# Kernel tuning notes

Measured on AMD Instinct MI355X. Metric: run time of the kernel, lower is better.

Reference implementation:

```python
import jax, jax.numpy as jnp
import numpy as np

DT = 1.0
EPS = 1e-12
BETA_MIN = 1e-4

def setup_inputs() -> dict:
    key = jax.random.key(0)
    k1, k2 = jax.random.split(key, 2)
    B, W, M, F = 32, 32, 4096, 8
    H = 256
    feature = jax.random.uniform(k1, (B, W, M, F), jnp.float32) * 1000.0
    N = jax.random.uniform(k2, (M,), jnp.float32, minval=1e5, maxval=1e6)
    # tanh-reparam params: (tanh(x)+1)/2 = p  ->  x = atanh(2p-1)
    logbeta = jnp.asarray(np.arctanh(2.0 * 0.3 - 1.0), jnp.float32)
    loggamma = jnp.asarray(np.arctanh(2.0 * 0.1 - 1.0), jnp.float32)
    return {"feature": feature, "logbeta": logbeta, "loggamma": loggamma, "N": N, "H": H}

def reference(feature, logbeta, loggamma, N, H):
    # feature: [B,W,M,F]; N: [M]; logbeta/loggamma: scalars; H: int horizon
    beta = (jnp.tanh(logbeta) + 1.0) * 0.5
    gamma = (jnp.tanh(loggamma) + 1.0) * 0.5
    B, W, M, F = feature.shape
    C0 = jnp.maximum(feature[:, -1, :, 0], 0.0)            # [B,M] latest observed incidence
    N_bm = jnp.broadcast_to(N[None, :], (B, M))            # [B,M]
    beta_safe = jnp.maximum(beta, BETA_MIN)
    I0 = jnp.clip(C0 / beta_safe, 0.0, N_bm)
    S0 = jnp.maximum(N_bm - I0, 0.0)                       # R0 = 0 (learn_r0_frac=False)
    state0 = jnp.stack([S0, I0, jnp.zeros_like(I0)], axis=-1)  # [B,M,3]

    def step(state, _):
        S, I = state[..., 0], state[..., 1]
        inc = beta * S * I / (N_bm + EPS)                  # new infections per step
        c_step = DT * inc                                  # obs == 'incidence'
        dstate = jnp.stack([-inc, inc - gamma * I, gamma * I], axis=-1)
        new = jnp.maximum(state + DT * dstate, 0.0)
        total = new.sum(axis=-1, keepdims=True)            # enforce_mass
        new = new * (N_bm[..., None] / (total + EPS))
        return new, c_step

    _, cases = jax.lax.scan(step, state0, None, length=H)  # cases: [H,B,M]
    return jnp.transpose(cases, (1, 0, 2))                 # [B,H,M]
```

## Files before the change

### kernel.cpp

```cpp
#include <hip/hip_runtime.h>
#include <hip/hip_bf16.h>

#define DT_C   1.0f
#define EPS_C  1e-12f
#define BETA_MIN_C 1e-4f

__global__ void __launch_bounds__(256)
sir_rollout_kernel(const float* __restrict__ feature,
                   const float* __restrict__ logbeta,
                   const float* __restrict__ loggamma,
                   const float* __restrict__ Nvec,
                   float* __restrict__ out,
                   int B, int W, int M, int F, int H) {
    const int idx = blockIdx.x * blockDim.x + threadIdx.x;
    if (idx >= B * M) return;
    const int b = idx / M;
    const int m = idx - b * M;

    const float beta  = (tanhf(logbeta[0])  + 1.0f) * 0.5f;
    const float gamma = (tanhf(loggamma[0]) + 1.0f) * 0.5f;
    const float beta_safe = fmaxf(beta, BETA_MIN_C);

    const float n = Nvec[m];
    const float binv = beta / (n + EPS_C);

    const size_t fidx = ((size_t)(b * W + (W - 1)) * (size_t)M + (size_t)m) * (size_t)F;
    const float c0 = fmaxf(feature[fidx], 0.0f);

    float I = fminf(fmaxf(c0 / beta_safe, 0.0f), n);
    float S = fmaxf(n - I, 0.0f);
    float R = 0.0f;

    float* o = out + (size_t)b * (size_t)H * (size_t)M + (size_t)m;
    const size_t ostride = (size_t)M;

    #pragma unroll 4
    for (int h = 0; h < H; ++h) {
        const float inc = S * I * binv;
        o[(size_t)h * ostride] = inc;

        const float gI = gamma * I;
        const float nS = fmaxf(S - inc, 0.0f);
        const float nI = fmaxf(I + (inc - gI), 0.0f);
        const float nR = fmaxf(R + gI, 0.0f);

        const float t  = (nS + nI + nR) + EPS_C;
        float r = __builtin_amdgcn_rcpf(t);
        r = r + r * fmaf(-t, r, 1.0f);
        const float scale = n * r;

        S = nS * scale;
        I = nI * scale;
        R = nR * scale;
    }
}

extern "C" void kernel_launch(void* const* d_in, const int* in_sizes, int n_in,
                              void* d_out, int out_size, void* d_ws, size_t ws_size,
                              hipStream_t stream) {
    const float* feature  = (const float*)d_in[0];
    const float* logbeta  = (const float*)d_in[1];
    const float* loggamma = (const float*)d_in[2];
    const float* Nvec     = (const float*)d_in[3];
    float* out = (float*)d_out;

    const int M = in_sizes[3];
    const int B = 32;
    const int F = 8;
    const int W = in_sizes[0] / (B * M * F);
    const int H = out_size / (B * M);

    const int nthreads = B * M;
    const int block = 256;
    const int grid = (nthreads + block - 1) / block;

    sir_rollout_kernel<<<grid, block, 0, stream>>>(feature, logbeta, loggamma,
                                                   Nvec, out, B, W, M, F, H);
}
```

Before: 207.4 us.

## Stage incidence outputs in LDS and emit vectorized float4 stores per chunk

Each thread now computes eight time steps into a double-buffered LDS tile. After a block barrier, the tile is written to global memory with float4 stores instead of one scalar store per step. The aim is fewer, wider global store instructions. In exchange it adds LDS traffic, a __syncthreads per chunk and extra address arithmetic, inside a serial, latency-bound recurrence that runs at low occupancy.

After: 209.7 us. No clear change (+1.1%).

```diff
diff --git a/kernel.cpp b/kernel.cpp
--- a/kernel.cpp
+++ b/kernel.cpp
@@ -1,57 +1,106 @@
 #include <hip/hip_runtime.h>
-#include <hip/hip_bf16.h>
 
 #define DT_C   1.0f
 #define EPS_C  1e-12f
 #define BETA_MIN_C 1e-4f
+#define HCHUNK 8
+#define BLK 256
 
-__global__ void __launch_bounds__(256)
+__global__ void __launch_bounds__(BLK)
 sir_rollout_kernel(const float* __restrict__ feature,
                    const float* __restrict__ logbeta,
                    const float* __restrict__ loggamma,
                    const float* __restrict__ Nvec,
                    float* __restrict__ out,
                    int B, int W, int M, int F, int H) {
-    const int idx = blockIdx.x * blockDim.x + threadIdx.x;
-    if (idx >= B * M) return;
-    const int b = idx / M;
-    const int m = idx - b * M;
+    __shared__ float lds[2][HCHUNK][BLK];
+
+    const int tid       = threadIdx.x;
+    const int blockBase = blockIdx.x * BLK;
+    const int idx       = blockBase + tid;
+    const int total     = B * M;
+    const bool active   = (idx < total);
 
     const float beta  = (tanhf(logbeta[0])  + 1.0f) * 0.5f;
     const float gamma = (tanhf(loggamma[0]) + 1.0f) * 0.5f;
     const float beta_safe = fmaxf(beta, BETA_MIN_C);
 
-    const float n = Nvec[m];
-    const float binv = beta / (n + EPS_C);
+    float n = 0.0f, binv = 0.0f, S = 0.0f, I = 0.0f, R = 0.0f;
+    if (active) {
+        const int b = idx / M;
+        const int m = idx - b * M;
+        n    = Nvec[m];
+        binv = beta / (n + EPS_C);
+        const size_t fidx = ((size_t)(b * W + (W - 1)) * (size_t)M + (size_t)m) * (size_t)F;
+        const float c0 = fmaxf(feature[fidx], 0.0f);
+        I = fminf(fmaxf(c0 / beta_safe, 0.0f), n);
+        S = fmaxf(n - I, 0.0f);
+        R = 0.0f;
+    }
 
-    const size_t fidx = ((size_t)(b * W + (W - 1)) * (size_t)M + (size_t)m) * (size_t)F;
-    const float c0 = fmaxf(feature[fidx], 0.0f);
+    const int hc_count = H / HCHUNK;
+    int buf = 0;
 
-    float I = fminf(fmaxf(c0 / beta_safe, 0.0f), n);
-    float S = fmaxf(n - I, 0.0f);
-    float R = 0.0f;
+    for (int hc = 0; hc < hc_count; ++hc) {
+        #pragma unroll
+        for (int j = 0; j < HCHUNK; ++j) {
+            const float inc = S * I * binv;
+            lds[buf][j][tid] = inc;
 
-    float* o = out + (size_t)b * (size_t)H * (size_t)M + (size_t)m;
-    const size_t ostride = (size_t)M;
+            const float gI = gamma * I;
+            const float nS = fmaxf(S - inc, 0.0f);
+            const float nI = fmaxf(I + (inc - gI), 0.0f);
+            const float nR = fmaxf(R + gI, 0.0f);
 
-    #pragma unroll 4
-    for (int h = 0; h < H; ++h) {
-        const float inc = S * I * binv;
-        o[(size_t)h * ostride] = inc;
+            const float t  = (nS + nI + nR) + EPS_C;
+            float r = __builtin_amdgcn_rcpf(t);
+            r = r + r * fmaf(-t, r, 1.0f);
+            const float scale = n * r;
 
-        const float gI = gamma * I;
-        const float nS = fmaxf(S - inc, 0.0f);
-        const float nI = fmaxf(I + (inc - gI), 0.0f);
-        const float nR = fmaxf(R + gI, 0.0f);
+            S = nS * scale;
+            I = nI * scale;
+            R = nR * scale;
+        }
 
-        const float t  = (nS + nI + nR) + EPS_C;
-        float r = __builtin_amdgcn_rcpf(t);
-        r = r + r * fmaf(-t, r, 1.0f);
-        const float scale = n * r;
+        __syncthreads();
 
-        S = nS * scale;
-        I = nI * scale;
-        R = nR * scale;
+        const int hbase = hc * HCHUNK;
+        #pragma unroll
+        for (int k = 0; k < 2; ++k) {
+            const int q    = tid + k * BLK;
+            const int j    = q >> 6;
+            const int c4   = (q & 63) << 2;
+            const int gidx = blockBase + c4;
+            if (gidx + 3 < total) {
+                const int bq = gidx / M;
+                const int mq = gidx - bq * M;
+                const float4 v = *reinterpret_cast<const float4*>(&lds[buf][j][c4]);
+                *reinterpret_cast<float4*>(
+                    out + ((size_t)bq * (size_t)H + (size_t)(hbase + j)) * (size_t)M + (size_t)mq) = v;
+            }
+        }
+        buf ^= 1;
+    }
+
+    if (active) {
+        const int b = idx / M;
+        const int m = idx - b * M;
+        float* o = out + (size_t)b * (size_t)H * (size_t)M + (size_t)m;
+        for (int h = hc_count * HCHUNK; h < H; ++h) {
+            const float inc = S * I * binv;
+            o[(size_t)h * (size_t)M] = inc;
+            const float gI = gamma * I;
+            const float nS = fmaxf(S - inc, 0.0f);
+            const float nI = fmaxf(I + (inc - gI), 0.0f);
+            const float nR = fmaxf(R + gI, 0.0f);
+            const float t  = (nS + nI + nR) + EPS_C;
+            float r = __builtin_amdgcn_rcpf(t);
+            r = r + r * fmaf(-t, r, 1.0f);
+            const float scale = n * r;
+            S = nS * scale;
+            I = nI * scale;
+            R = nR * scale;
+        }
     }
 }
 
@@ -71,9 +120,8 @@
     const int H = out_size / (B * M);
 
     const int nthreads = B * M;
-    const int block = 256;
-    const int grid = (nthreads + block - 1) / block;
+    const int grid = (nthreads + BLK - 1) / BLK;
 
-    sir_rollout_kernel<<<grid, block, 0, stream>>>(feature, logbeta, loggamma,
-                                                   Nvec, out, B, W, M, F, H);
+    sir_rollout_kernel<<<grid, BLK, 0, stream>>>(feature, logbeta, loggamma,
+                                                 Nvec, out, B, W, M, F, H);
 }
```
